# Kernel optimization log

Measured on AMD Instinct MI355X. Metric: run time of the kernel, lower is better.

Reference implementation:

```python
import jax, jax.numpy as jnp
import numpy as np

IN_CH, OUT_CH, SUPPORT = 128, 128, 3
BS, N = 8, 2048


def knn_idx(x, k):
    # x: (bs, n, d) -> (bs, n, k) indices of k nearest (excluding self)
    sq = jnp.sum(x * x, axis=-1)  # (bs, n)
    dist = sq[:, :, None] + sq[:, None, :] - 2.0 * jnp.einsum('bnd,bmd->bnm', x, x)
    _, idx = jax.lax.top_k(-dist, k + 1)  # smallest distances
    return idx[:, :, 1:]


def gather_neighbors(t, idx):
    # t: (bs, n, d), idx: (bs, n, k) -> (bs, n, k, d)
    return jax.vmap(lambda tb, ib: tb[ib])(t, idx)


def l2_normalize(x, axis, eps=1e-12):
    n = jnp.linalg.norm(x, axis=axis, keepdims=True)
    return x / jnp.maximum(n, eps)


def setup_inputs() -> dict:
    key = jax.random.key(0)
    ks = jax.random.split(key, 8)
    stdv = 1.0 / np.sqrt(OUT_CH * (SUPPORT + 1))
    return {
        'vertices': jax.random.normal(ks[0], (BS, N, 3), jnp.float32),
        'feature_map': jax.random.normal(ks[1], (BS, N, IN_CH), jnp.float32),
        'weights': jax.random.uniform(ks[2], (IN_CH, (SUPPORT + 1) * OUT_CH), jnp.float32, -stdv, stdv),
        'bias': jax.random.uniform(ks[3], ((SUPPORT + 1) * OUT_CH,), jnp.float32, -stdv, stdv),
        'directions': jax.random.uniform(ks[4], (3, SUPPORT * OUT_CH), jnp.float32, -stdv, stdv),
        'ste_w': jax.random.normal(ks[5], (OUT_CH, IN_CH), jnp.float32) * (1.0 / np.sqrt(IN_CH)),
        'conv2_w': jax.random.normal(ks[6], (OUT_CH, 2 * OUT_CH), jnp.float32) * (1.0 / np.sqrt(2 * OUT_CH)),
        'neighbor_num': 16,
    }


def reference(vertices, feature_map, weights, bias, directions, ste_w, conv2_w, neighbor_num):
    bs, n, _ = vertices.shape
    k = neighbor_num

    # STE branch: 1x1 conv == per-point linear
    f_ste = jnp.einsum('bnc,oc->bno', feature_map, ste_w)

    # Receptive fields: KNN in feature space ('RF-F'), directions from vertices
    neighbor_index = knn_idx(feature_map, k)                      # (bs, n, k)
    neighbors = gather_neighbors(vertices, neighbor_index)        # (bs, n, k, 3)
    rf_norm = l2_normalize(neighbors - vertices[:, :, None, :], axis=-1)

    # Graph convolution (3D-GCN style)
    sdn = l2_normalize(directions, axis=0)                        # (3, s*out)
    theta = jax.nn.relu(jnp.einsum('bnkd,dm->bnkm', rf_norm, sdn))  # (bs,n,k,s*out)
    fm = feature_map @ weights + bias                             # (bs,n,(s+1)*out)
    feature_center = fm[:, :, :OUT_CH]
    feature_support = gather_neighbors(fm[:, :, OUT_CH:], neighbor_index)  # (bs,n,k,s*out)
    act = (theta * feature_support).reshape(bs, n, k, SUPPORT, OUT_CH)
    act = jnp.max(act, axis=2)          # max over neighbors
    act = jnp.mean(act, axis=2)         # mean over supports
    feature = feature_center + act      # (bs, n, out)

    # ORL: global context via point-space KNN max-pool
    nb_idx2 = knn_idx(vertices, k)
    pooled = jnp.max(gather_neighbors(feature, nb_idx2), axis=2)  # (bs,n,out)
    f_global = jnp.broadcast_to(jnp.mean(pooled, axis=1, keepdims=True), (bs, n, OUT_CH))
    feat_cat = jnp.concatenate([feature, f_global], axis=-1)      # (bs,n,2*out)
    feature_fuse = jnp.einsum('bnc,oc->bno', feat_cat, conv2_w) + feature

    return feature_fuse + f_ste
```

## Files before the change

### kernel.cpp

```cpp
#include <hip/hip_runtime.h>
#include <hip/hip_bf16.h>

#define BS 8
#define NP 2048
#define CIN 128
#define OC 128
#define NSUP 3
#define KNN 16
#define NC 512
#define SC 384
#define CAND 24

typedef __attribute__((ext_vector_type(8))) short bf16x8;
typedef __attribute__((ext_vector_type(4))) float f32x4;

__device__ inline unsigned short f2bf(float x) {
    __hip_bfloat16 h = __float2bfloat16(x);
    return *reinterpret_cast<unsigned short*>(&h);
}
__device__ inline unsigned fkey(float d, int gi) {
    unsigned u = __float_as_uint(d);
    u ^= (unsigned)((int)u >> 31) | 0x80000000u;
    return (u & 0xFFFFF800u) | (unsigned)gi;
}
__device__ inline unsigned umn(unsigned a, unsigned b) { return a < b ? a : b; }
__device__ inline unsigned umx(unsigned a, unsigned b) { return a > b ? a : b; }
__device__ inline unsigned dpp_prev(unsigned v) {
    return (unsigned)__builtin_amdgcn_update_dpp(0, (int)v, 0x111, 0xF, 0xF, true);
}

__global__ __launch_bounds__(256) void prep_kernel(const float* __restrict__ in,
                                                   float* __restrict__ sq,
                                                   short* __restrict__ outp,
                                                   const float* __restrict__ W,
                                                   const float* __restrict__ conv2,
                                                   const float* __restrict__ stew,
                                                   const float* __restrict__ dirs,
                                                   short* __restrict__ Wt,
                                                   short* __restrict__ conv2b,
                                                   short* __restrict__ stewb,
                                                   float4* __restrict__ sdnn4) {
    const int tid = threadIdx.x;
    if (blockIdx.x < 1024) {
        const int row = blockIdx.x * 16 + (tid >> 4);
        const int seg = tid & 15;
        const float* p = in + (size_t)row * CIN + seg * 8;
        float4 f0 = *(const float4*)p;
        float4 f1 = *(const float4*)(p + 4);
        bf16x8 s;
        s[0] = (short)f2bf(f0.x); s[1] = (short)f2bf(f0.y);
        s[2] = (short)f2bf(f0.z); s[3] = (short)f2bf(f0.w);
        s[4] = (short)f2bf(f1.x); s[5] = (short)f2bf(f1.y);
        s[6] = (short)f2bf(f1.z); s[7] = (short)f2bf(f1.w);
        *(bf16x8*)&outp[(size_t)row * CIN + seg * 8] = s;
        float ss = f0.x*f0.x + f0.y*f0.y + f0.z*f0.z + f0.w*f0.w
                 + f1.x*f1.x + f1.y*f1.y + f1.z*f1.z + f1.w*f1.w;
#pragma unroll
        for (int msk = 1; msk <= 8; msk <<= 1) ss += __shfl_xor(ss, msk);
        if (seg == 0) sq[row] = ss;
    } else if (blockIdx.x < 1472) {
        int idx = (blockIdx.x - 1024) * 256 + tid;
        if (idx < NC * CIN) {
            int n = idx >> 7, k = idx & 127;
            Wt[idx] = (short)f2bf(W[(size_t)k * NC + n]);
        } else if (idx < NC * CIN + OC * 2 * OC) {
            int e = idx - NC * CIN;
            conv2b[e] = (short)f2bf(conv2[e]);
        } else {
            int e = idx - NC * CIN - OC * 2 * OC;
            stewb[e] = (short)f2bf(stew[e]);
        }
    } else {
        int m = (blockIdx.x - 1472) * 256 + tid;
        if (m < SC) {
            float d0 = dirs[m], d1 = dirs[SC + m], d2 = dirs[2 * SC + m];
            float nrm = sqrtf(d0 * d0 + d1 * d1 + d2 * d2);
            float den = fmaxf(nrm, 1e-12f);
            sdnn4[m] = make_float4(d0 / den, d1 / den, d2 / den, 0.f);
        }
    }
}

#define TQF 32
#define TPF 64
#define NCHF (NP / TPF)
__global__ __launch_bounds__(256) void knn_feat_kernel(const short* __restrict__ fbb,
                                                       const float* __restrict__ sqn,
                                                       int* __restrict__ cand) {
    __shared__ alignas(16) short Qb[TQF][128];
    __shared__ alignas(16) short Pb[TPF][128];
    __shared__ float sqP[TPF];
    __shared__ unsigned Ds[TQF][68];

    const int b = blockIdx.y, q0 = blockIdx.x * TQF, tid = threadIdx.x;
    const int lane = tid & 63, wid = tid >> 6;
    const short* fb = fbb + (size_t)b * NP * CIN;

    unsigned l0 = 0xFFFFFFFFu, l1 = 0xFFFFFFFFu, l2 = 0xFFFFFFFFu;
    unsigned T = 0xFFFFFFFFu;
    const int gbase = lane & 56;
    const int sub = lane & 7;

    for (int i = 0; i < 2; ++i) {
        int v = i * 256 + tid, row = v >> 4, g = v & 15;
        *(bf16x8*)&Qb[row][(g ^ (row & 7)) * 8] =
            *(const bf16x8*)&fb[(size_t)(q0 + row) * CIN + g * 8];
    }
    for (int i = 0; i < 4; ++i) {
        int v = i * 256 + tid, row = v >> 4, g = v & 15;
        *(bf16x8*)&Pb[row][(g ^ (row & 7)) * 8] =
            *(const bf16x8*)&fb[(size_t)row * CIN + g * 8];
    }
    if (tid < TPF) sqP[tid] = sqn[b * NP + tid];

    const int qt = wid >> 1, ph = wid & 1;
    const int qsl = tid >> 3;
    const int arow = qt * 16 + (lane & 15), asw = arow & 7;
    const int brow0 = ph * 32 + (lane & 15), brow1 = brow0 + 16;
    const int bsw0 = brow0 & 7, bsw1 = brow1 & 7;
    const int oct = lane >> 4;
    const int qrow = qt * 16 + oct * 4;

    for (int ch = 0; ch < NCHF; ++ch) {
        __syncthreads();
        bf16x8 st0, st1, st2, st3;
        float sq_next = 0.f;
        const int nxt = (ch + 1 < NCHF);
        if (nxt) {
            int p0n = (ch + 1) * TPF;
            { int v = tid;       int row = v>>4, g = v&15; st0 = *(const bf16x8*)&fb[(size_t)(p0n+row)*CIN + g*8]; }
            { int v = 256 + tid; int row = v>>4, g = v&15; st1 = *(const bf16x8*)&fb[(size_t)(p0n+row)*CIN + g*8]; }
            { int v = 512 + tid; int row = v>>4, g = v&15; st2 = *(const bf16x8*)&fb[(size_t)(p0n+row)*CIN + g*8]; }
            { int v = 768 + tid; int row = v>>4, g = v&15; st3 = *(const bf16x8*)&fb[(size_t)(p0n+row)*CIN + g*8]; }
            if (tid < TPF) sq_next = sqn[b * NP + p0n + tid];
        }
        f32x4 acc0 = {0.f,0.f,0.f,0.f}, acc1 = {0.f,0.f,0.f,0.f};
#pragma unroll
        for (int kk = 0; kk < 4; ++kk) {
            int g = kk * 4 + oct;
            bf16x8 av  = *(const bf16x8*)&Qb[arow][(g ^ asw) * 8];
            bf16x8 bv0 = *(const bf16x8*)&Pb[brow0][(g ^ bsw0) * 8];
            bf16x8 bv1 = *(const bf16x8*)&Pb[brow1][(g ^ bsw1) * 8];
            acc0 = __builtin_amdgcn_mfma_f32_16x16x32_bf16(av, bv0, acc0, 0, 0, 0);
            acc1 = __builtin_amdgcn_mfma_f32_16x16x32_bf16(av, bv1, acc1, 0, 0, 0);
        }
        const float sp0 = sqP[brow0], sp1 = sqP[brow1];
        const int pg0 = ch * TPF + brow0, pg1 = ch * TPF + brow1;
#pragma unroll
        for (int r = 0; r < 4; ++r) {
            int qg = q0 + qrow + r;
            unsigned k0 = fkey(sp0 - 2.0f * acc0[r], pg0);
            unsigned k1 = fkey(sp1 - 2.0f * acc1[r], pg1);
            if (qg == pg0) k0 = 0xFFFFFFFFu;
            if (qg == pg1) k1 = 0xFFFFFFFFu;
            Ds[qrow + r][brow0] = k0;
            Ds[qrow + r][brow1] = k1;
        }
        __syncthreads();

        {
            uint4 kA = *(const uint4*)&Ds[qsl][sub * 8];
            uint4 kB = *(const uint4*)&Ds[qsl][sub * 8 + 4];
            unsigned kv[8] = {kA.x, kA.y, kA.z, kA.w, kB.x, kB.y, kB.z, kB.w};
#pragma unroll
            for (int j = 0; j < 8; ++j) {
                unsigned long long bal = __ballot(kv[j] < T);
                unsigned gm = (unsigned)(bal >> gbase) & 0xFFu;
                while (gm) {
                    int l = __builtin_ctz(gm);
                    gm &= gm - 1;
                    unsigned k = (unsigned)__shfl((int)kv[j], gbase + l);
                    unsigned pv = dpp_prev(l2);
                    if (sub == 0) pv = 0u;
                    unsigned n0 = umn(umx(pv, k), l0);
                    unsigned n1 = umn(umx(l0, k), l1);
                    unsigned n2 = umn(umx(l1, k), l2);
                    l0 = n0; l1 = n1; l2 = n2;
                }
            }
            T = (unsigned)__shfl((int)l2, gbase + 7);
        }
        if (nxt) {
            { int v = tid;       int row = v>>4, g = v&15; *(bf16x8*)&Pb[row][(g^(row&7))*8] = st0; }
            { int v = 256 + tid; int row = v>>4, g = v&15; *(bf16x8*)&Pb[row][(g^(row&7))*8] = st1; }
            { int v = 512 + tid; int row = v>>4, g = v&15; *(bf16x8*)&Pb[row][(g^(row&7))*8] = st2; }
            { int v = 768 + tid; int row = v>>4, g = v&15; *(bf16x8*)&Pb[row][(g^(row&7))*8] = st3; }
            if (tid < TPF) sqP[tid] = sq_next;
        }
    }

    {
        int* dst = cand + ((size_t)b * NP + q0 + qsl) * CAND;
        dst[3 * sub + 0] = (int)(l0 & 0x7FFu);
        dst[3 * sub + 1] = (int)(l1 & 0x7FFu);
        dst[3 * sub + 2] = (int)(l2 & 0x7FFu);
    }
}

__global__ __launch_bounds__(256) void knn_refine_kernel(const float* __restrict__ feat,
                                                         const int* __restrict__ cand,
                                                         int* __restrict__ nbr) {
    __shared__ unsigned long long keyS[4][CAND];
    const int w = threadIdx.x >> 6;
    const int lane = threadIdx.x & 63;
    const int grp = lane >> 4, sl = lane & 15;
    const int gq = blockIdx.x * 4 + w;
    const int b = gq >> 11;
    const int q = gq & (NP - 1);
    const float* fb = feat + (size_t)b * NP * CIN;

    double qd[8];
    {
        float4 a = *(const float4*)&fb[(size_t)q * CIN + sl * 8];
        float4 c = *(const float4*)&fb[(size_t)q * CIN + sl * 8 + 4];
        qd[0] = a.x; qd[1] = a.y; qd[2] = a.z; qd[3] = a.w;
        qd[4] = c.x; qd[5] = c.y; qd[6] = c.z; qd[7] = c.w;
    }
    double sqd = 0.0;
#pragma unroll
    for (int i = 0; i < 8; ++i) sqd += qd[i] * qd[i];
#pragma unroll
    for (int msk = 1; msk <= 8; msk <<= 1) sqd += __shfl_xor(sqd, msk);
    const float sqi = (float)sqd;

    const int* cq = cand + (size_t)gq * CAND;
    int jv[CAND / 4];
#pragma unroll
    for (int t = 0; t < CAND / 4; ++t) jv[t] = cq[t * 4 + grp];

#pragma unroll
    for (int t = 0; t < CAND / 4; ++t) {
        const int j = jv[t];
        float4 a = *(const float4*)&fb[(size_t)j * CIN + sl * 8];
        float4 c = *(const float4*)&fb[(size_t)j * CIN + sl * 8 + 4];
        double fd[8] = {a.x, a.y, a.z, a.w, c.x, c.y, c.z, c.w};
        double dot = 0.0, sj = 0.0;
#pragma unroll
        for (int i = 0; i < 8; ++i) { dot += qd[i] * fd[i]; sj += fd[i] * fd[i]; }
#pragma unroll
        for (int msk = 1; msk <= 8; msk <<= 1) {
            dot += __shfl_xor(dot, msk);
            sj  += __shfl_xor(sj, msk);
        }
        if (sl == 0) {
            float t1 = sqi + (float)sj;
            float t2 = (float)(2.0 * dot);
            float d32 = t1 - t2;
            unsigned u = __float_as_uint(d32);
            u ^= (unsigned)((int)u >> 31) | 0x80000000u;
            keyS[w][t * 4 + grp] = ((unsigned long long)u << 32) | (unsigned)j;
        }
    }
    __syncthreads();
    if (lane < CAND) {
        unsigned long long k = keyS[w][lane];
        int rank = 0;
#pragma unroll
        for (int m = 0; m < CAND; ++m) rank += (keyS[w][m] < k) ? 1 : 0;
        if (rank < KNN) nbr[(size_t)gq * KNN + rank] = (int)(k & 0xFFFFFFFFu);
    }
}

#define TQV 32
__global__ __launch_bounds__(256) void knn_vert_kernel(const float* __restrict__ vert,
                                                       int* __restrict__ nbr) {
    __shared__ alignas(16) float vx[NP], vy[NP], vz[NP];
    const int b = blockIdx.y;
    const int q0 = blockIdx.x * TQV;
    const int tid = threadIdx.x;
    const float* vb = vert + (size_t)b * NP * 3;

    for (int i = 0; i < NP * 3 / 256; ++i) {
        int e = i * 256 + tid;
        float v = vb[e];
        int row = e / 3, comp = e % 3;
        (comp == 0 ? vx : comp == 1 ? vy : vz)[row] = v;
    }
    __syncthreads();

    const int lane = tid & 63;
    const int gbase = lane & 56;
    const int q = tid >> 3;
    const int sub = tid & 7;
    const float qx = vx[q0 + q], qy = vy[q0 + q], qz = vz[q0 + q];

    unsigned l0 = 0xFFFFFFFFu, l1 = 0xFFFFFFFFu, l2 = 0xFFFFFFFFu;
    unsigned T = 0xFFFFFFFFu;

    for (int m = 0; m < NP / 64; ++m) {
        const int p0 = m * 64 + sub * 8;
        float4 xA = *(const float4*)&vx[p0], xB = *(const float4*)&vx[p0 + 4];
        float4 yA = *(const float4*)&vy[p0], yB = *(const float4*)&vy[p0 + 4];
        float4 zA = *(const float4*)&vz[p0], zB = *(const float4*)&vz[p0 + 4];
        float dv[8];
        { float dx = qx-xA.x, dy = qy-yA.x, dz = qz-zA.x; dv[0] = dx*dx+dy*dy+dz*dz; }
        { float dx = qx-xA.y, dy = qy-yA.y, dz = qz-zA.y; dv[1] = dx*dx+dy*dy+dz*dz; }
        { float dx = qx-xA.z, dy = qy-yA.z, dz = qz-zA.z; dv[2] = dx*dx+dy*dy+dz*dz; }
        { float dx = qx-xA.w, dy = qy-yA.w, dz = qz-zA.w; dv[3] = dx*dx+dy*dy+dz*dz; }
        { float dx = qx-xB.x, dy = qy-yB.x, dz = qz-zB.x; dv[4] = dx*dx+dy*dy+dz*dz; }
        { float dx = qx-xB.y, dy = qy-yB.y, dz = qz-zB.y; dv[5] = dx*dx+dy*dy+dz*dz; }
        { float dx = qx-xB.z, dy = qy-yB.z, dz = qz-zB.z; dv[6] = dx*dx+dy*dy+dz*dz; }
        { float dx = qx-xB.w, dy = qy-yB.w, dz = qz-zB.w; dv[7] = dx*dx+dy*dy+dz*dz; }
        unsigned kv[8];
#pragma unroll
        for (int j = 0; j < 8; ++j) kv[j] = fkey(dv[j], p0 + j);
#pragma unroll
        for (int j = 0; j < 8; ++j) {
            unsigned long long bal = __ballot(kv[j] < T);
            unsigned gm = (unsigned)(bal >> gbase) & 0xFFu;
            while (gm) {
                int l = __builtin_ctz(gm);
                gm &= gm - 1;
                unsigned k = (unsigned)__shfl((int)kv[j], gbase + l);
                unsigned pv = dpp_prev(l2);
                if (sub == 0) pv = 0u;
                unsigned n0 = umn(umx(pv, k), l0);
                unsigned n1 = umn(umx(l0, k), l1);
                unsigned n2 = umn(umx(l1, k), l2);
                l0 = n0; l1 = n1; l2 = n2;
            }
        }
        T = (unsigned)__shfl((int)l2, gbase + 7);
    }
    {
        int* dst = nbr + ((size_t)b * NP + q0 + q) * KNN;
        unsigned vals[3] = {l0, l1, l2};
#pragma unroll
        for (int e = 0; e < 3; ++e) {
            int r = 3 * sub + e;
            if (r >= 1 && r <= 16) dst[r - 1] = (int)(vals[e] & 0x7FFu);
        }
    }
}

__global__ __launch_bounds__(256) void fm_gemm_kernel(const short* __restrict__ fbb,
                                                      const short* __restrict__ Wt,
                                                      const float* __restrict__ bias,
                                                      float* __restrict__ C) {
    __shared__ alignas(16) short As[64][128];
    const int m0 = blockIdx.x * 64, n0 = blockIdx.y * 128, tid = threadIdx.x;
    const int lane = tid & 63, wid = tid >> 6, oct = lane >> 4;
    for (int i = 0; i < 4; ++i) {
        int v = i * 256 + tid, row = v >> 4, g = v & 15;
        *(bf16x8*)&As[row][(g ^ (row & 7)) * 8] =
            *(const bf16x8*)&fbb[(size_t)(m0 + row) * CIN + g * 8];
    }
    __syncthreads();
    f32x4 acc[4][2] = {};
#pragma unroll
    for (int kk = 0; kk < 4; ++kk) {
        int g = kk * 4 + oct;
        bf16x8 bv[2];
#pragma unroll
        for (int nt = 0; nt < 2; ++nt) {
            int n = n0 + (wid * 2 + nt) * 16 + (lane & 15);
            bv[nt] = *(const bf16x8*)&Wt[(size_t)n * CIN + g * 8];
        }
#pragma unroll
        for (int mt = 0; mt < 4; ++mt) {
            int ar = mt * 16 + (lane & 15);
            bf16x8 av = *(const bf16x8*)&As[ar][(g ^ (ar & 7)) * 8];
#pragma unroll
            for (int nt = 0; nt < 2; ++nt)
                acc[mt][nt] = __builtin_amdgcn_mfma_f32_16x16x32_bf16(av, bv[nt], acc[mt][nt], 0, 0, 0);
        }
    }
#pragma unroll
    for (int mt = 0; mt < 4; ++mt)
#pragma unroll
        for (int nt = 0; nt < 2; ++nt) {
            int n = n0 + (wid * 2 + nt) * 16 + (lane & 15);
            float bsv = bias[n];
            int mbase = m0 + mt * 16 + oct * 4;
#pragma unroll
            for (int r = 0; r < 4; ++r)
                C[(size_t)(mbase + r) * NC + n] = acc[mt][nt][r] + bsv;
        }
}

__global__ __launch_bounds__(128) void act_kernel(const float* __restrict__ fm,
                                                  const int* __restrict__ nbr,
                                                  const float* __restrict__ vert,
                                                  const float4* __restrict__ sdnn4,
                                                  float* __restrict__ feature,
                                                  short* __restrict__ featb) {
    __shared__ int sj[KNN];
    __shared__ float rf[KNN][4];
    const int i = blockIdx.x;
    const int b = blockIdx.y;
    const int tid = threadIdx.x;
    const size_t bi = (size_t)b * NP + i;
    if (tid < KNN) {
        int j = nbr[bi * KNN + tid];
        sj[tid] = j;
        const float* vb = vert + (size_t)b * NP * 3;
        float dx = vb[j * 3 + 0] - vb[i * 3 + 0];
        float dy = vb[j * 3 + 1] - vb[i * 3 + 1];
        float dz = vb[j * 3 + 2] - vb[i * 3 + 2];
        float nrm = sqrtf(dx * dx + dy * dy + dz * dz);
        float den = fmaxf(nrm, 1e-12f);
        rf[tid][0] = dx / den; rf[tid][1] = dy / den; rf[tid][2] = dz / den;
    }
    __syncthreads();
    const int oc = tid;
    float accm = 0.0f;
#pragma unroll
    for (int s = 0; s < NSUP; ++s) {
        int m = s * OC + oc;
        float4 sv = sdnn4[m];
        float s0 = sv.x, s1 = sv.y, s2 = sv.z;
        float vm[4] = {-3.0e38f, -3.0e38f, -3.0e38f, -3.0e38f};
#pragma unroll
        for (int kk = 0; kk < KNN; ++kk) {
            float th = fmaxf(rf[kk][0] * s0 + rf[kk][1] * s1 + rf[kk][2] * s2, 0.0f);
            float sup = fm[((size_t)b * NP + sj[kk]) * NC + OC + m];
            vm[kk & 3] = fmaxf(vm[kk & 3], th * sup);
        }
        accm += fmaxf(fmaxf(vm[0], vm[1]), fmaxf(vm[2], vm[3]));
    }
    float v = fm[bi * NC + oc] + accm / 3.0f;
    feature[bi * OC + oc] = v;
    featb[bi * OC + oc] = (short)f2bf(v);
}

__global__ __launch_bounds__(128) void pool_kernel(const float* __restrict__ feature,
                                                   const int* __restrict__ nbr2,
                                                   float* __restrict__ pooled) {
    __shared__ int sj[KNN];
    const int i = blockIdx.x, b = blockIdx.y, tid = threadIdx.x;
    const size_t bi = (size_t)b * NP + i;
    if (tid < KNN) sj[tid] = nbr2[bi * KNN + tid];
    __syncthreads();
    float m0 = -3.0e38f, m1 = -3.0e38f, m2 = -3.0e38f, m3 = -3.0e38f;
#pragma unroll
    for (int kk = 0; kk < KNN; kk += 4) {
        m0 = fmaxf(m0, feature[((size_t)b * NP + sj[kk + 0]) * OC + tid]);
        m1 = fmaxf(m1, feature[((size_t)b * NP + sj[kk + 1]) * OC + tid]);
        m2 = fmaxf(m2, feature[((size_t)b * NP + sj[kk + 2]) * OC + tid]);
        m3 = fmaxf(m3, feature[((size_t)b * NP + sj[kk + 3]) * OC + tid]);
    }
    pooled[bi * OC + tid] = fmaxf(fmaxf(m0, m1), fmaxf(m2, m3));
}

__global__ __launch_bounds__(128) void partial_kernel(const float* __restrict__ pooled,
                                                      float* __restrict__ part) {
    const int ch = blockIdx.x, b = blockIdx.y, tid = threadIdx.x;
    float s0 = 0.f, s1 = 0.f, s2 = 0.f, s3 = 0.f;
    const float* base = pooled + ((size_t)b * NP + ch * 128) * OC + tid;
    for (int i = 0; i < 128; i += 4) {
        s0 += base[(size_t)(i + 0) * OC];
        s1 += base[(size_t)(i + 1) * OC];
        s2 += base[(size_t)(i + 2) * OC];
        s3 += base[(size_t)(i + 3) * OC];
    }
    part[((size_t)b * 16 + ch) * OC + tid] = ((s0 + s1) + (s2 + s3));
}
__global__ __launch_bounds__(128) void fg_gdot_kernel(const float* __restrict__ part,
                                                      const float* __restrict__ conv2,
                                                      float* __restrict__ gd) {
    __shared__ float fgs[OC];
    const int b = blockIdx.x, tid = threadIdx.x;
    float s = 0.f;
#pragma unroll
    for (int c = 0; c < 16; ++c) s += part[((size_t)b * 16 + c) * OC + tid];
    fgs[tid] = s / (float)NP;
    __syncthreads();
    float g = 0.f;
    const float* w = conv2 + (size_t)tid * 2 * OC + OC;
    for (int c = 0; c < OC; ++c) g += fgs[c] * w[c];
    gd[b * OC + tid] = g;
}

__global__ __launch_bounds__(256) void final_kernel(const short* __restrict__ featb,
                                                    const short* __restrict__ fbb,
                                                    const short* __restrict__ conv2b,
                                                    const short* __restrict__ stewb,
                                                    const float* __restrict__ gd,
                                                    const float* __restrict__ feature,
                                                    float* __restrict__ out) {
    __shared__ alignas(16) short Af[32][128];
    __shared__ alignas(16) short Am[32][128];
    const int m0 = blockIdx.x * 32, tid = threadIdx.x;
    const int lane = tid & 63, wid = tid >> 6, oct = lane >> 4;
    for (int i = 0; i < 2; ++i) {
        int v = i * 256 + tid, row = v >> 4, g = v & 15;
        *(bf16x8*)&Af[row][(g ^ (row & 7)) * 8] =
            *(const bf16x8*)&featb[(size_t)(m0 + row) * OC + g * 8];
        *(bf16x8*)&Am[row][(g ^ (row & 7)) * 8] =
            *(const bf16x8*)&fbb[(size_t)(m0 + row) * CIN + g * 8];
    }
    __syncthreads();
    f32x4 acc[2][2] = {};
#pragma unroll
    for (int kk = 0; kk < 4; ++kk) {
        int g = kk * 4 + oct;
        bf16x8 bC[2], bS[2];
#pragma unroll
        for (int nt = 0; nt < 2; ++nt) {
            int n = (wid * 2 + nt) * 16 + (lane & 15);
            bC[nt] = *(const bf16x8*)&conv2b[(size_t)n * (2 * OC) + g * 8];
            bS[nt] = *(const bf16x8*)&stewb[(size_t)n * CIN + g * 8];
        }
#pragma unroll
        for (int mt = 0; mt < 2; ++mt) {
            int ar = mt * 16 + (lane & 15);
            bf16x8 aF = *(const bf16x8*)&Af[ar][(g ^ (ar & 7)) * 8];
            bf16x8 aM = *(const bf16x8*)&Am[ar][(g ^ (ar & 7)) * 8];
#pragma unroll
            for (int nt = 0; nt < 2; ++nt) {
                acc[mt][nt] = __builtin_amdgcn_mfma_f32_16x16x32_bf16(aF, bC[nt], acc[mt][nt], 0, 0, 0);
                acc[mt][nt] = __builtin_amdgcn_mfma_f32_16x16x32_bf16(aM, bS[nt], acc[mt][nt], 0, 0, 0);
            }
        }
    }
#pragma unroll
    for (int mt = 0; mt < 2; ++mt)
#pragma unroll
        for (int nt = 0; nt < 2; ++nt) {
            int o = (wid * 2 + nt) * 16 + (lane & 15);
            int mbase = m0 + mt * 16 + oct * 4;
#pragma unroll
            for (int r = 0; r < 4; ++r) {
                int m = mbase + r;
                out[(size_t)m * OC + o] = acc[mt][nt][r]
                    + gd[(m >> 11) * OC + o] + feature[(size_t)m * OC + o];
            }
        }
}

extern "C" void kernel_launch(void* const* d_in, const int* in_sizes, int n_in,
                              void* d_out, int out_size, void* d_ws, size_t ws_size,
                              hipStream_t stream) {
    const float* vert  = (const float*)d_in[0];
    const float* fmap  = (const float*)d_in[1];
    const float* W     = (const float*)d_in[2];
    const float* bias  = (const float*)d_in[3];
    const float* dirs  = (const float*)d_in[4];
    const float* stew  = (const float*)d_in[5];
    const float* conv2 = (const float*)d_in[6];
    float* out = (float*)d_out;

    float* ws      = (float*)d_ws;
    float* sqn     = ws;
    short* fbb     = (short*)(sqn + 16384);
    float* C1      = sqn + 16384 + 1048576;
    float* feature = C1 + 8388608;
    short* featb   = (short*)(feature + 2097152);
    float* gd      = feature + 2097152 + 1048576;
    short* Wt      = (short*)(gd + 1024);
    short* conv2b  = Wt + 65536;
    short* stewb   = conv2b + 32768;
    int*   nbr1    = (int*)(stewb + 16384);
    int*   nbr2    = nbr1 + 262144;
    float* part    = (float*)(nbr2 + 262144);
    float4* sdnn4  = (float4*)(part + 16384);
    int*   cand    = (int*)C1;
    float* pooled  = C1;

    prep_kernel<<<1474, 256, 0, stream>>>(fmap, sqn, fbb, W, conv2, stew, dirs,
                                          Wt, conv2b, stewb, sdnn4);
    knn_feat_kernel<<<dim3(64, 8), 256, 0, stream>>>(fbb, sqn, cand);
    knn_refine_kernel<<<4096, 256, 0, stream>>>(fmap, cand, nbr1);
    knn_vert_kernel<<<dim3(64, 8), 256, 0, stream>>>(vert, nbr2);
    fm_gemm_kernel<<<dim3(256, 4), 256, 0, stream>>>(fbb, Wt, bias, C1);
    act_kernel<<<dim3(2048, 8), 128, 0, stream>>>(C1, nbr1, vert, sdnn4, feature, featb);
    pool_kernel<<<dim3(2048, 8), 128, 0, stream>>>(feature, nbr2, pooled);
    partial_kernel<<<dim3(16, 8), 128, 0, stream>>>(pooled, part);
    fg_gdot_kernel<<<8, 128, 0, stream>>>(part, conv2, gd);
    final_kernel<<<512, 256, 0, stream>>>(featb, fbb, conv2b, stewb, gd, feature, out);
}
```

Measured before the change: 221.6 us.

## Seed KNN thresholds early and store support features and pooling input in bf16

Two unrelated changes are bundled. In both KNN kernels, the first chunk seeds the selection threshold from a sorting network's third-smallest key reduced across 8 lanes, so fewer early candidates go through the serial insertion loop. The GEMM epilogue now writes center features in fp32 and support features as bf16 into separate buffers, and the act and pool kernels gather bf16 data, which halves gather traffic at some precision cost. The workspace layout is rearranged so the candidate and pooled buffers no longer alias the old C1 buffer.

```diff
diff --git a/kernel.cpp b/kernel.cpp
--- a/kernel.cpp
+++ b/kernel.cpp
@@ -18,6 +18,10 @@
     __hip_bfloat16 h = __float2bfloat16(x);
     return *reinterpret_cast<unsigned short*>(&h);
 }
+__device__ inline float bf2f(short s) {
+    unsigned u = ((unsigned)(unsigned short)s) << 16;
+    return __uint_as_float(u);
+}
 __device__ inline unsigned fkey(float d, int gi) {
     unsigned u = __float_as_uint(d);
     u ^= (unsigned)((int)u >> 31) | 0x80000000u;
@@ -25,8 +29,22 @@
 }
 __device__ inline unsigned umn(unsigned a, unsigned b) { return a < b ? a : b; }
 __device__ inline unsigned umx(unsigned a, unsigned b) { return a > b ? a : b; }
+__device__ inline void cswap(unsigned& a, unsigned& b) {
+    unsigned t = umn(a, b); b = umx(a, b); a = t;
+}
 __device__ inline unsigned dpp_prev(unsigned v) {
     return (unsigned)__builtin_amdgcn_update_dpp(0, (int)v, 0x111, 0xF, 0xF, true);
+}
+__device__ inline unsigned third_smallest8(const unsigned kv[8]) {
+    unsigned s0=kv[0],s1=kv[1],s2=kv[2],s3=kv[3],s4=kv[4],s5=kv[5],s6=kv[6],s7=kv[7];
+    cswap(s0,s1); cswap(s2,s3); cswap(s4,s5); cswap(s6,s7);
+    cswap(s0,s2); cswap(s1,s3); cswap(s4,s6); cswap(s5,s7);
+    cswap(s1,s2); cswap(s5,s6); cswap(s0,s4); cswap(s3,s7);
+    cswap(s1,s5); cswap(s2,s6);
+    cswap(s1,s4); cswap(s3,s6);
+    cswap(s2,s4); cswap(s3,s5);
+    cswap(s3,s4);
+    return s2;
 }
 
 __global__ __launch_bounds__(256) void prep_kernel(const float* __restrict__ in,
@@ -162,6 +180,13 @@
             uint4 kA = *(const uint4*)&Ds[qsl][sub * 8];
             uint4 kB = *(const uint4*)&Ds[qsl][sub * 8 + 4];
             unsigned kv[8] = {kA.x, kA.y, kA.z, kA.w, kB.x, kB.y, kB.z, kB.w};
+            if (ch == 0) {
+                unsigned m3 = third_smallest8(kv);
+                m3 = umx(m3, (unsigned)__shfl_xor((int)m3, 1));
+                m3 = umx(m3, (unsigned)__shfl_xor((int)m3, 2));
+                m3 = umx(m3, (unsigned)__shfl_xor((int)m3, 4));
+                T = m3 + 1;
+            }
 #pragma unroll
             for (int j = 0; j < 8; ++j) {
                 unsigned long long bal = __ballot(kv[j] < T);
@@ -304,6 +329,13 @@
         unsigned kv[8];
 #pragma unroll
         for (int j = 0; j < 8; ++j) kv[j] = fkey(dv[j], p0 + j);
+        if (m == 0) {
+            unsigned m3 = third_smallest8(kv);
+            m3 = umx(m3, (unsigned)__shfl_xor((int)m3, 1));
+            m3 = umx(m3, (unsigned)__shfl_xor((int)m3, 2));
+            m3 = umx(m3, (unsigned)__shfl_xor((int)m3, 4));
+            T = m3 + 1;
+        }
 #pragma unroll
         for (int j = 0; j < 8; ++j) {
             unsigned long long bal = __ballot(kv[j] < T);
@@ -336,7 +368,8 @@
 __global__ __launch_bounds__(256) void fm_gemm_kernel(const short* __restrict__ fbb,
                                                       const short* __restrict__ Wt,
                                                       const float* __restrict__ bias,
-                                                      float* __restrict__ C) {
+                                                      float* __restrict__ centerf,
+                                                      short* __restrict__ supb) {
     __shared__ alignas(16) short As[64][128];
     const int m0 = blockIdx.x * 64, n0 = blockIdx.y * 128, tid = threadIdx.x;
     const int lane = tid & 63, wid = tid >> 6, oct = lane >> 4;
@@ -373,12 +406,18 @@
             float bsv = bias[n];
             int mbase = m0 + mt * 16 + oct * 4;
 #pragma unroll
-            for (int r = 0; r < 4; ++r)
-                C[(size_t)(mbase + r) * NC + n] = acc[mt][nt][r] + bsv;
-        }
-}
-
-__global__ __launch_bounds__(128) void act_kernel(const float* __restrict__ fm,
+            for (int r = 0; r < 4; ++r) {
+                float val = acc[mt][nt][r] + bsv;
+                if (n0 == 0)
+                    centerf[(size_t)(mbase + r) * OC + n] = val;
+                else
+                    supb[(size_t)(mbase + r) * SC + (n - OC)] = (short)f2bf(val);
+            }
+        }
+}
+
+__global__ __launch_bounds__(128) void act_kernel(const float* __restrict__ centerf,
+                                                  const short* __restrict__ supb,
                                                   const int* __restrict__ nbr,
                                                   const float* __restrict__ vert,
                                                   const float4* __restrict__ sdnn4,
@@ -413,17 +452,17 @@
 #pragma unroll
         for (int kk = 0; kk < KNN; ++kk) {
             float th = fmaxf(rf[kk][0] * s0 + rf[kk][1] * s1 + rf[kk][2] * s2, 0.0f);
-            float sup = fm[((size_t)b * NP + sj[kk]) * NC + OC + m];
+            float sup = bf2f(supb[((size_t)b * NP + sj[kk]) * SC + m]);
             vm[kk & 3] = fmaxf(vm[kk & 3], th * sup);
         }
         accm += fmaxf(fmaxf(vm[0], vm[1]), fmaxf(vm[2], vm[3]));
     }
-    float v = fm[bi * NC + oc] + accm / 3.0f;
+    float v = centerf[bi * OC + oc] + accm / 3.0f;
     feature[bi * OC + oc] = v;
     featb[bi * OC + oc] = (short)f2bf(v);
 }
 
-__global__ __launch_bounds__(128) void pool_kernel(const float* __restrict__ feature,
+__global__ __launch_bounds__(128) void pool_kernel(const short* __restrict__ featb,
                                                    const int* __restrict__ nbr2,
                                                    float* __restrict__ pooled) {
     __shared__ int sj[KNN];
@@ -434,10 +473,10 @@
     float m0 = -3.0e38f, m1 = -3.0e38f, m2 = -3.0e38f, m3 = -3.0e38f;
 #pragma unroll
     for (int kk = 0; kk < KNN; kk += 4) {
-        m0 = fmaxf(m0, feature[((size_t)b * NP + sj[kk + 0]) * OC + tid]);
-        m1 = fmaxf(m1, feature[((size_t)b * NP + sj[kk + 1]) * OC + tid]);
-        m2 = fmaxf(m2, feature[((size_t)b * NP + sj[kk + 2]) * OC + tid]);
-        m3 = fmaxf(m3, feature[((size_t)b * NP + sj[kk + 3]) * OC + tid]);
+        m0 = fmaxf(m0, bf2f(featb[((size_t)b * NP + sj[kk + 0]) * OC + tid]));
+        m1 = fmaxf(m1, bf2f(featb[((size_t)b * NP + sj[kk + 1]) * OC + tid]));
+        m2 = fmaxf(m2, bf2f(featb[((size_t)b * NP + sj[kk + 2]) * OC + tid]));
+        m3 = fmaxf(m3, bf2f(featb[((size_t)b * NP + sj[kk + 3]) * OC + tid]));
     }
     pooled[bi * OC + tid] = fmaxf(fmaxf(m0, m1), fmaxf(m2, m3));
 }
@@ -543,8 +582,9 @@
     float* ws      = (float*)d_ws;
     float* sqn     = ws;
     short* fbb     = (short*)(sqn + 16384);
-    float* C1      = sqn + 16384 + 1048576;
-    float* feature = C1 + 8388608;
+    float* centerf = sqn + 16384 + 1048576;
+    short* supb    = (short*)(centerf + 2097152);
+    float* feature = centerf + 2097152 + 3145728;
     short* featb   = (short*)(feature + 2097152);
     float* gd      = feature + 2097152 + 1048576;
     short* Wt      = (short*)(gd + 1024);
@@ -554,17 +594,18 @@
     int*   nbr2    = nbr1 + 262144;
     float* part    = (float*)(nbr2 + 262144);
     float4* sdnn4  = (float4*)(part + 16384);
-    int*   cand    = (int*)C1;
-    float* pooled  = C1;
+    int*   cand    = (int*)(sdnn4 + 384);
+    float* pooled  = (float*)(cand + 393216);
 
     prep_kernel<<<1474, 256, 0, stream>>>(fmap, sqn, fbb, W, conv2, stew, dirs,
                                           Wt, conv2b, stewb, sdnn4);
     knn_feat_kernel<<<dim3(64, 8), 256, 0, stream>>>(fbb, sqn, cand);
     knn_refine_kernel<<<4096, 256, 0, stream>>>(fmap, cand, nbr1);
     knn_vert_kernel<<<dim3(64, 8), 256, 0, stream>>>(vert, nbr2);
-    fm_gemm_kernel<<<dim3(256, 4), 256, 0, stream>>>(fbb, Wt, bias, C1);
-    act_kernel<<<dim3(2048, 8), 128, 0, stream>>>(C1, nbr1, vert, sdnn4, feature, featb);
-    pool_kernel<<<dim3(2048, 8), 128, 0, stream>>>(feature, nbr2, pooled);
+    fm_gemm_kernel<<<dim3(256, 4), 256, 0, stream>>>(fbb, Wt, bias, centerf, supb);
+    act_kernel<<<dim3(2048, 8), 128, 0, stream>>>(centerf, supb, nbr1, vert, sdnn4,
+                                                  feature, featb);
+    pool_kernel<<<dim3(2048, 8), 128, 0, stream>>>(featb, nbr2, pooled);
     partial_kernel<<<dim3(16, 8), 128, 0, stream>>>(pooled, part);
     fg_gdot_kernel<<<8, 128, 0, stream>>>(part, conv2, gd);
     final_kernel<<<512, 256, 0, stream>>>(featb, fbb, conv2b, stewb, gd, feature, out);
```

New measurement: 220.9 us. No clear change (-0.3%).
